# Kernel optimization log

Measured on AMD Instinct MI355X. Metric: run time of the kernel, lower is better.

The kernel has to match this reference:

```python
import jax, jax.numpy as jnp
import numpy as np

WS = 7   # window size
NH = 6   # num heads

def layer_norm(x, g, b, eps=1e-5):
    m = x.mean(-1, keepdims=True)
    v = ((x - m) ** 2).mean(-1, keepdims=True)
    return (x - m) / jnp.sqrt(v + eps) * g + b

def rel_pos_index(ws):
    coords = np.stack(np.meshgrid(np.arange(ws), np.arange(ws), indexing='ij')).reshape(2, -1)
    rel = (coords[:, :, None] - coords[:, None, :]).transpose(1, 2, 0)
    rel[:, :, 0] += ws - 1
    rel[:, :, 1] += ws - 1
    rel[:, :, 0] *= 2 * ws - 1
    return rel.sum(-1)  # (ws*ws, ws*ws) numpy int

RPI = rel_pos_index(WS)

def window_partition(x, ws):
    B, H, W, C = x.shape
    return x.reshape(B, H // ws, ws, W // ws, ws, C).transpose(0, 1, 3, 2, 4, 5).reshape(-1, ws * ws, C)

def window_reverse(w, ws, B, H, W):
    return w.reshape(B, H // ws, W // ws, ws, ws, -1).transpose(0, 1, 3, 2, 4, 5).reshape(B, H, W, -1)

def make_attn_mask(H, W, ws, shift):
    # Swin shifted-window mask (constant, computed in numpy)
    img = np.zeros((1, H, W, 1), np.float32)
    cnt = 0
    for h in (slice(0, -ws), slice(-ws, -shift), slice(-shift, None)):
        for w in (slice(0, -ws), slice(-ws, -shift), slice(-shift, None)):
            img[:, h, w, :] = cnt
            cnt += 1
    mw = img.reshape(1, H // ws, ws, W // ws, ws, 1).transpose(0, 1, 3, 2, 4, 5).reshape(-1, ws * ws)
    m = mw[:, None, :] - mw[:, :, None]
    return jnp.asarray(np.where(m != 0, -100.0, 0.0).astype(np.float32))  # (nW, N, N)

def conv2d(x, w, b, padding):
    y = jax.lax.conv_general_dilated(x, w, (1, 1), padding, dimension_numbers=('NCHW', 'OIHW', 'NCHW'))
    return y + b[None, :, None, None]

def swin_block(x, H, W, shift, n1g, n1b, qkvw, qkvb, projw, projb, rel, n2g, n2b, f1w, f1b, f2w, f2b):
    B, L, C = x.shape
    hd = C // NH
    shortcut = x
    x = layer_norm(x, n1g, n1b).reshape(B, H, W, C)
    if shift > 0:
        x = jnp.roll(x, (-shift, -shift), axis=(1, 2))
    xw = window_partition(x, WS)            # (B*nW, N, C)
    nWB, N, _ = xw.shape
    qkv = (xw @ qkvw.T + qkvb).reshape(nWB, N, 3, NH, hd).transpose(2, 0, 3, 1, 4)
    q, k, v = qkv[0] * (hd ** -0.5), qkv[1], qkv[2]
    attn = jnp.einsum('whnd,whmd->whnm', q, k)
    attn = attn + rel[RPI].transpose(2, 0, 1)[None]   # relative position bias (NH,N,N)
    if shift > 0:
        mask = make_attn_mask(H, W, WS, shift)        # (nW, N, N)
        nW = mask.shape[0]
        attn = (attn.reshape(B, nW, NH, N, N) + mask[None, :, None]).reshape(nWB, NH, N, N)
    attn = jax.nn.softmax(attn, axis=-1)
    xw = jnp.einsum('whnm,whmd->wnhd', attn, v).reshape(nWB, N, C)
    xw = xw @ projw.T + projb
    x = window_reverse(xw, WS, B, H, W)
    if shift > 0:
        x = jnp.roll(x, (shift, shift), axis=(1, 2))
    x = shortcut + x.reshape(B, L, C)
    h = layer_norm(x, n2g, n2b)
    h = jax.nn.gelu(h @ f1w.T + f1b, approximate=False) @ f2w.T + f2b
    return x + h

def setup_inputs() -> dict:
    key = jax.random.key(0)
    ks = iter(jax.random.split(key, 32))
    B, C, H, W = 8, 192, 56, 56
    C2, hid = C // 2, 4 * (C // 2)
    rn = lambda shape, s=0.02: jax.random.normal(next(ks), shape, jnp.float32) * s
    return dict(
        x=jax.random.normal(next(ks), (B, C, H, W), jnp.float32),
        up_w=rn((C2, C, 3, 3)), up_b=jnp.zeros((C2,), jnp.float32),
        bn_g=jnp.ones((C2,), jnp.float32), bn_b=jnp.zeros((C2,), jnp.float32),
        bn_mean=jnp.zeros((C2,), jnp.float32), bn_var=jnp.ones((C2,), jnp.float32),
        n1g=jnp.ones((2, C2), jnp.float32), n1b=jnp.zeros((2, C2), jnp.float32),
        qkv_w=rn((2, 3 * C2, C2)), qkv_b=jnp.zeros((2, 3 * C2), jnp.float32),
        proj_w=rn((2, C2, C2)), proj_b=jnp.zeros((2, C2), jnp.float32),
        rel=rn((2, (2 * WS - 1) ** 2, NH)),
        n2g=jnp.ones((2, C2), jnp.float32), n2b=jnp.zeros((2, C2), jnp.float32),
        f1w=rn((2, hid, C2)), f1b=jnp.zeros((2, hid), jnp.float32),
        f2w=rn((2, C2, hid)), f2b=jnp.zeros((2, C2), jnp.float32),
        out_w=rn((C // 4, C2, 1, 1)), out_b=jnp.zeros((C // 4,), jnp.float32),
    )

def reference(x, up_w, up_b, bn_g, bn_b, bn_mean, bn_var, n1g, n1b, qkv_w, qkv_b, proj_w, proj_b, rel, n2g, n2b, f1w, f1b, f2w, f2b, out_w, out_b):
    B, C, H, W = x.shape
    x = jnp.repeat(jnp.repeat(x, 2, axis=2), 2, axis=3)
    x = conv2d(x, up_w, up_b, 'SAME')
    x = (x - bn_mean[None, :, None, None]) * (bn_g / jnp.sqrt(bn_var + 1e-5))[None, :, None, None] + bn_b[None, :, None, None]
    x = jax.nn.relu(x)
    H2, W2, C2 = 2 * H, 2 * W, C // 2
    t = x.reshape(B, C2, H2 * W2).transpose(0, 2, 1)   # (B, L, C2)
    for i, shift in enumerate((0, WS // 2)):
        t = swin_block(t, H2, W2, shift, n1g[i], n1b[i], qkv_w[i], qkv_b[i], proj_w[i], proj_b[i], rel[i], n2g[i], n2b[i], f1w[i], f1b[i], f2w[i], f2b[i])
    x = t.transpose(0, 2, 1).reshape(B, C2, H2, W2)
    return jax.nn.relu(conv2d(x, out_w, out_b, 'VALID'))
```

## Files before the change

### kernel.cpp

```cpp
#include <hip/hip_runtime.h>
#include <math.h>

#define M_TOK 100352
#define NHEAD 6

typedef unsigned short u16;
typedef __attribute__((ext_vector_type(8))) short bf16x8;
typedef __attribute__((ext_vector_type(4))) float f32x4;
typedef __attribute__((ext_vector_type(4))) unsigned int u32x4;

__device__ inline float bf2f(u16 u) {
    union { float f; unsigned int i; } v; v.i = ((unsigned int)u) << 16; return v.f;
}
__device__ inline u16 f2bf(float f) {
    union { float f; unsigned int i; } v; v.f = f;
    unsigned int r = v.i + 0x7fffu + ((v.i >> 16) & 1u);
    return (u16)(r >> 16);
}

__global__ __launch_bounds__(256) void cast_w_kernel(const float* __restrict__ qkvw,
        const float* __restrict__ projw, const float* __restrict__ f1w,
        const float* __restrict__ f2w, u16* __restrict__ Wh) {
    int i = blockIdx.x * 256 + threadIdx.x;
    if (i < 55296) Wh[i] = f2bf(qkvw[i]);
    else if (i < 73728) Wh[i] = f2bf(projw[i - 55296]);
    else if (i < 147456) Wh[i] = f2bf(f1w[i - 73728]);
    else if (i < 221184) Wh[i] = f2bf(f2w[i - 147456]);
}

__global__ __launch_bounds__(256) void fold_kernel(const float* __restrict__ up_w,
                                                   u16* __restrict__ Wc) {
    int idx = blockIdx.x * 256 + threadIdx.x;
    if (idx >= 96 * 4 * 192) return;
    int c2 = idx / 768;
    int rem = idx - c2 * 768;
    int p = rem / 192;
    int ci = rem - p * 192;
    int po = p >> 1, pw = p & 1;
    const float* w = up_w + (c2 * 192 + ci) * 9;
    float w9[9];
#pragma unroll
    for (int k = 0; k < 9; k++) w9[k] = w[k];
    float r0[3], r1[3];
#pragma unroll
    for (int kw = 0; kw < 3; kw++) {
        if (po == 0) { r0[kw] = w9[kw];              r1[kw] = w9[3 + kw] + w9[6 + kw]; }
        else         { r0[kw] = w9[kw] + w9[3 + kw]; r1[kw] = w9[6 + kw]; }
    }
    float o00, o01, o10, o11;
    if (pw == 0) { o00 = r0[0];         o01 = r0[1] + r0[2]; o10 = r1[0];         o11 = r1[1] + r1[2]; }
    else         { o00 = r0[0] + r0[1]; o01 = r0[2];         o10 = r1[0] + r1[1]; o11 = r1[2]; }
    size_t base = ((size_t)p * 4 * 96 + c2) * 192 + ci;
    Wc[base + 0 * 96 * 192] = f2bf(o00);
    Wc[base + 1 * 96 * 192] = f2bf(o01);
    Wc[base + 2 * 96 * 192] = f2bf(o10);
    Wc[base + 3 * 96 * 192] = f2bf(o11);
}

__global__ __launch_bounds__(256) void bias_gen(const float* __restrict__ rel,
                                                float* __restrict__ BT) {
    int blkid = blockIdx.x;
    int blk = blkid / 24;
    int rem = blkid - blk * 24;
    int type = rem / 6, head = rem - (rem / 6) * 6;
    const float* relp = rel + blk * 1014;
    bool shift = (blk == 1);
    for (int i = threadIdx.x; i < 4096; i += 256) {
        int a = i >> 6, k = i & 63;
        float v;
        if (k >= 49) v = -1e30f;
        else if (a >= 49) v = 0.f;
        else {
            int ah = (a * 37) >> 8, aw = a - ah * 7;
            int kh = (k * 37) >> 8, kw = k - kh * 7;
            v = relp[((ah - kh + 6) * 13 + (aw - kw + 6)) * 6 + head];
            if (shift) {
                int lha = (type & 2) ? (ah < 4 ? 1 : 2) : 0;
                int lwa = (type & 1) ? (aw < 4 ? 1 : 2) : 0;
                int lhk = (type & 2) ? (kh < 4 ? 1 : 2) : 0;
                int lwk = (type & 1) ? (kw < 4 ? 1 : 2) : 0;
                if (lha != lhk || lwa != lwk) v -= 100.f;
            }
        }
        BT[(size_t)blkid * 4096 + i] = v;
    }
}

__global__ __launch_bounds__(256) void transpose_kernel(const float* __restrict__ x,
                                                        u16* __restrict__ xT) {
    __shared__ unsigned int ts[64 * 96];
    int b = blockIdx.y;
    int pix0 = blockIdx.x * 64;
    int tid = threadIdx.x;
    int p = tid & 63, dg = tid >> 6;
    const float* xb = x + (size_t)b * 192 * 3136 + pix0 + p;
    for (int d = dg; d < 96; d += 4) {
        float v0 = xb[(size_t)(2 * d) * 3136];
        float v1 = xb[(size_t)(2 * d + 1) * 3136];
        unsigned int pk = ((unsigned int)f2bf(v1) << 16) | (unsigned int)f2bf(v0);
        ts[p * 96 + ((d & ~31) | ((d & 31) ^ (p & 31)))] = pk;
    }
    __syncthreads();
    for (int i = tid; i < 1536; i += 256) {
        int pp = i / 24, c = i - pp * 24;
        unsigned int r[4];
#pragma unroll
        for (int j = 0; j < 4; j++) {
            int d = c * 4 + j;
            r[j] = ts[pp * 96 + ((d & ~31) | ((d & 31) ^ (pp & 31)))];
        }
        u32x4 v = {r[0], r[1], r[2], r[3]};
        *(u32x4*)&xT[((size_t)b * 3136 + pix0 + pp) * 192 + c * 8] = v;
    }
}

__global__ __launch_bounds__(256) void conv_mfma(const u16* __restrict__ xT,
        const u16* __restrict__ Wc, const float* __restrict__ up_b,
        const float* __restrict__ bn_g, const float* __restrict__ bn_b,
        const float* __restrict__ bn_m, const float* __restrict__ bn_v,
        float* __restrict__ T) {
    __shared__ u16 xs[81 * 200];
    __shared__ u16 ws[96 * 104];
    int tile = blockIdx.x, p = blockIdx.y, b = blockIdx.z;
    int po = p >> 1, pw = p & 1;
    int a0 = (tile / 7) * 8, b0 = (tile % 7) * 8;
    int rro = a0 - 1 + po, cco = b0 - 1 + pw;
    int tid = threadIdx.x;
    int w = tid >> 6, lane = tid & 63, quad = lane >> 4, l16 = lane & 15;
    int mbase = (w & 1) * 32;
    int nt0 = (w >> 1) * 3;

    for (int i = tid; i < 1944; i += 256) {
        int pix = i / 24, c = i - pix * 24;
        int rr = pix / 9, cc = pix - rr * 9;
        int gr = rro + rr, gc = cco + cc;
        u32x4 v = {0u, 0u, 0u, 0u};
        if ((unsigned)gr < 56u && (unsigned)gc < 56u)
            v = *(const u32x4*)&xT[((size_t)b * 3136 + gr * 56 + gc) * 192 + c * 8];
        *(u32x4*)&xs[pix * 200 + c * 8] = v;
    }

    f32x4 zero = {0.f, 0.f, 0.f, 0.f};
    f32x4 acc[2][3];
#pragma unroll
    for (int mi = 0; mi < 2; mi++)
#pragma unroll
        for (int ni = 0; ni < 3; ni++) acc[mi][ni] = zero;

    int aoffp[2];
#pragma unroll
    for (int mi = 0; mi < 2; mi++) {
        int pixel = mbase + mi * 16 + l16;
        aoffp[mi] = ((pixel >> 3) * 9 + (pixel & 7)) * 200;
    }

    for (int tap = 0; tap < 4; tap++) {
        int di = tap >> 1, dj = tap & 1;
        int tsh = (di * 9 + dj) * 200;
        for (int kc = 0; kc < 2; kc++) {
            __syncthreads();
            for (int i = tid; i < 1152; i += 256) {
                int r = i / 12, c = i - r * 12;
                *(u32x4*)&ws[r * 104 + c * 8] =
                    *(const u32x4*)&Wc[(((size_t)p * 4 + tap) * 96 + r) * 192 + kc * 96 + c * 8];
            }
            __syncthreads();
#pragma unroll
            for (int kk = 0; kk < 3; kk++) {
                bf16x8 af[2], bfr[3];
#pragma unroll
                for (int mi = 0; mi < 2; mi++)
                    af[mi] = *(const bf16x8*)&xs[aoffp[mi] + tsh + kc * 96 + kk * 32 + quad * 8];
#pragma unroll
                for (int ni = 0; ni < 3; ni++)
                    bfr[ni] = *(const bf16x8*)&ws[((nt0 + ni) * 16 + l16) * 104 + kk * 32 + quad * 8];
#pragma unroll
                for (int mi = 0; mi < 2; mi++)
#pragma unroll
                    for (int ni = 0; ni < 3; ni++)
                        acc[mi][ni] = __builtin_amdgcn_mfma_f32_16x16x32_bf16(
                            af[mi], bfr[ni], acc[mi][ni], 0, 0, 0);
            }
        }
    }

#pragma unroll
    for (int ni = 0; ni < 3; ni++) {
        int c2 = (nt0 + ni) * 16 + l16;
        float sc = bn_g[c2] * rsqrtf(bn_v[c2] + 1e-5f);
        float sh = (up_b[c2] - bn_m[c2]) * sc + bn_b[c2];
#pragma unroll
        for (int mi = 0; mi < 2; mi++) {
#pragma unroll
            for (int reg = 0; reg < 4; reg++) {
                int pixel = mbase + mi * 16 + quad * 4 + reg;
                int pr = pixel >> 3, pc = pixel & 7;
                int oh = 2 * (a0 + pr) + po, ow = 2 * (b0 + pc) + pw;
                size_t tok = (size_t)b * 12544 + oh * 112 + ow;
                T[tok * 96 + c2] = fmaxf(acc[mi][ni][reg] * sc + sh, 0.f);
            }
        }
    }
}

__global__ __launch_bounds__(256) void ln_kernel(const float* __restrict__ X,
        const float* __restrict__ g, const float* __restrict__ bta,
        u16* __restrict__ Y) {
    int tok = blockIdx.x * 4 + (threadIdx.x >> 6);
    int lane = threadIdx.x & 63;
    const float* row = X + (size_t)tok * 96;
    float x1 = row[lane];
    float x2 = (lane < 32) ? row[64 + lane] : 0.f;
    float s = x1 + x2, q = x1 * x1 + x2 * x2;
#pragma unroll
    for (int off = 32; off; off >>= 1) {
        s += __shfl_xor(s, off, 64);
        q += __shfl_xor(q, off, 64);
    }
    float mean = s * (1.f / 96.f);
    float var = q * (1.f / 96.f) - mean * mean;
    float rstd = rsqrtf(var + 1e-5f);
    u16* outp = Y + (size_t)tok * 96;
    outp[lane] = f2bf((x1 - mean) * rstd * g[lane] + bta[lane]);
    if (lane < 32) outp[64 + lane] = f2bf((x2 - mean) * rstd * g[64 + lane] + bta[64 + lane]);
}

template <int EPI>
__global__ __launch_bounds__(256) void gemm_mfma(const u16* __restrict__ A,
        const u16* __restrict__ W, const float* __restrict__ bias,
        void* Cout, const float* res, int N, int K) {
    __shared__ u16 As[128 * 104];
    __shared__ u16 Bs[96 * 104];
    int tid = threadIdx.x;
    int w = tid >> 6, lane = tid & 63, quad = lane >> 4, l16 = lane & 15;
    int n0 = blockIdx.x * 96;
    size_t m0 = (size_t)blockIdx.y * 128;
    int mbase = (w & 1) * 64;
    int nt0 = (w >> 1) * 3;

    f32x4 zero = {0.f, 0.f, 0.f, 0.f};
    f32x4 acc[4][3];
#pragma unroll
    for (int mi = 0; mi < 4; mi++)
#pragma unroll
        for (int ni = 0; ni < 3; ni++) acc[mi][ni] = zero;

    for (int k0 = 0; k0 < K; k0 += 96) {
        __syncthreads();
        for (int i = tid; i < 1536; i += 256) {
            int r = i / 12, c = i - r * 12;
            *(u32x4*)&As[r * 104 + c * 8] = *(const u32x4*)&A[(m0 + r) * K + k0 + c * 8];
        }
        for (int i = tid; i < 1152; i += 256) {
            int r = i / 12, c = i - r * 12;
            *(u32x4*)&Bs[r * 104 + c * 8] = *(const u32x4*)&W[(size_t)(n0 + r) * K + k0 + c * 8];
        }
        __syncthreads();
#pragma unroll
        for (int kk = 0; kk < 3; kk++) {
            bf16x8 af[4], bfr[3];
#pragma unroll
            for (int mi = 0; mi < 4; mi++)
                af[mi] = *(const bf16x8*)&As[(mbase + mi * 16 + l16) * 104 + kk * 32 + quad * 8];
#pragma unroll
            for (int ni = 0; ni < 3; ni++)
                bfr[ni] = *(const bf16x8*)&Bs[((nt0 + ni) * 16 + l16) * 104 + kk * 32 + quad * 8];
#pragma unroll
            for (int mi = 0; mi < 4; mi++)
#pragma unroll
                for (int ni = 0; ni < 3; ni++)
                    acc[mi][ni] = __builtin_amdgcn_mfma_f32_16x16x32_bf16(
                        af[mi], bfr[ni], acc[mi][ni], 0, 0, 0);
        }
    }

#pragma unroll
    for (int ni = 0; ni < 3; ni++) {
        int col = n0 + (nt0 + ni) * 16 + l16;
        float bv = bias[col];
#pragma unroll
        for (int mi = 0; mi < 4; mi++) {
            size_t rowb = m0 + mbase + mi * 16 + quad * 4;
#pragma unroll
            for (int reg = 0; reg < 4; reg++) {
                size_t row = rowb + reg;
                float v = acc[mi][ni][reg] + bv;
                if (EPI == 1) v = 0.5f * v * (1.f + erff(v * 0.70710678118654752f));
                if (EPI == 2) {
                    v += res[row * N + col];
                    ((float*)Cout)[row * N + col] = v;
                } else {
                    ((u16*)Cout)[row * N + col] = f2bf(v);
                }
            }
        }
    }
}

__global__ __launch_bounds__(192, 3) void attn_mfma(const u16* __restrict__ qkv,
        const float* __restrict__ BT, u16* __restrict__ ao, int shift) {
    __shared__ u16 Pl[3][64 * 72];
    __shared__ u16 vts[3][16 * 72];

    int tid = threadIdx.x;
    int w = tid >> 6, lane = tid & 63, quad = lane >> 4, l16 = lane & 15;
    int Wd = blockIdx.x;
    int bb = Wd >> 8, wl = Wd & 255, wh = wl >> 4, ww = wl & 15;
    int type = ((wh == 15) ? 2 : 0) + ((ww == 15) ? 1 : 0);

    int toks4[4], tokV;
#pragma unroll
    for (int t = 0; t < 4; t++) {
        int a = t * 16 + l16; if (a > 48) a = 48;
        int r = (a * 37) >> 8, c = a - r * 7;
        int h = wh * 7 + r, wq = ww * 7 + c;
        if (shift) { h += 3; if (h >= 112) h -= 112; wq += 3; if (wq >= 112) wq -= 112; }
        toks4[t] = bb * 12544 + h * 112 + wq;
    }
    {
        int a = lane > 48 ? 48 : lane;
        int r = (a * 37) >> 8, c = a - r * 7;
        int h = wh * 7 + r, wq = ww * 7 + c;
        if (shift) { h += 3; if (h >= 112) h -= 112; wq += 3; if (wq >= 112) wq -= 112; }
        tokV = bb * 12544 + h * 112 + wq;
    }

    u16* Pw = Pl[w];
    u16* vw = vts[w];

    for (int i = lane; i < 240; i += 64) {
        int rrow = i / 15, key = 49 + (i - rrow * 15);
        vw[rrow * 72 + key] = 0;
    }

    for (int hh = 0; hh < 2; hh++) {
        int head = w * 2 + hh;

        union { u32x4 u; bf16x8 h; } qf[4], kf[4];
#pragma unroll
        for (int t = 0; t < 4; t++) {
            u32x4 zq = {0u, 0u, 0u, 0u}, zk = {0u, 0u, 0u, 0u};
            if (quad < 2) {
                const u16* rb = qkv + (size_t)toks4[t] * 288 + head * 16 + quad * 8;
                zq = *(const u32x4*)(rb);
                zk = *(const u32x4*)(rb + 96);
            }
            qf[t].u = zq; kf[t].u = zk;
        }

        if (lane < 49) {
            const u16* vb = qkv + (size_t)tokV * 288 + head * 16 + 192;
            union { u32x4 v; unsigned int u[4]; } v0, v1;
            v0.v = *(const u32x4*)(vb);
            v1.v = *(const u32x4*)(vb + 8);
#pragma unroll
            for (int j = 0; j < 4; j++) {
                vw[(2 * j) * 72 + lane]         = (u16)(v0.u[j] & 0xffffu);
                vw[(2 * j + 1) * 72 + lane]     = (u16)(v0.u[j] >> 16);
                vw[(8 + 2 * j) * 72 + lane]     = (u16)(v1.u[j] & 0xffffu);
                vw[(8 + 2 * j + 1) * 72 + lane] = (u16)(v1.u[j] >> 16);
            }
        }

        f32x4 S[4][4];
#pragma unroll
        for (int kt = 0; kt < 4; kt++)
#pragma unroll
            for (int qt = 0; qt < 4; qt++)
                S[kt][qt] = __builtin_amdgcn_mfma_f32_16x16x32_bf16(
                    kf[kt].h, qf[qt].h, f32x4{0.f, 0.f, 0.f, 0.f}, 0, 0, 0);

        const float* bbase = BT + (size_t)(type * 6 + head) * 4096;
        float rinv[4];
#pragma unroll
        for (int qt = 0; qt < 4; qt++) {
            f32x4 bv[4];
#pragma unroll
            for (int kt = 0; kt < 4; kt++)
                bv[kt] = *(const f32x4*)&bbase[(size_t)(qt * 16 + l16) * 64 + kt * 16 + quad * 4];
            float mx = -3e38f;
#pragma unroll
            for (int kt = 0; kt < 4; kt++)
#pragma unroll
                for (int r = 0; r < 4; r++) {
                    float v = fmaf(S[kt][qt][r], 0.25f, bv[kt][r]);
                    S[kt][qt][r] = v;
                    mx = fmaxf(mx, v);
                }
            mx = fmaxf(mx, __shfl_xor(mx, 16, 64));
            mx = fmaxf(mx, __shfl_xor(mx, 32, 64));
            float sm = 0.f;
#pragma unroll
            for (int kt = 0; kt < 4; kt++)
#pragma unroll
                for (int r = 0; r < 4; r++) {
                    float e = __expf(S[kt][qt][r] - mx);
                    S[kt][qt][r] = e;
                    sm += e;
                }
            sm += __shfl_xor(sm, 16, 64);
            sm += __shfl_xor(sm, 32, 64);
            rinv[qt] = 1.0f / sm;
        }

#pragma unroll
        for (int qt = 0; qt < 4; qt++)
#pragma unroll
            for (int kt = 0; kt < 4; kt++) {
                unsigned int d0 = ((unsigned int)f2bf(S[kt][qt][1]) << 16) | f2bf(S[kt][qt][0]);
                unsigned int d1 = ((unsigned int)f2bf(S[kt][qt][3]) << 16) | f2bf(S[kt][qt][2]);
                *(uint2*)&Pw[(qt * 16 + l16) * 72 + kt * 16 + quad * 4] = make_uint2(d0, d1);
            }

        bf16x8 vf[2];
#pragma unroll
        for (int ksp = 0; ksp < 2; ksp++)
            vf[ksp] = *(const bf16x8*)&vw[l16 * 72 + ksp * 32 + quad * 8];
#pragma unroll
        for (int qt = 0; qt < 4; qt++) {
            f32x4 O = {0.f, 0.f, 0.f, 0.f};
#pragma unroll
            for (int ksp = 0; ksp < 2; ksp++) {
                bf16x8 pf = *(const bf16x8*)&Pw[(qt * 16 + l16) * 72 + ksp * 32 + quad * 8];
                O = __builtin_amdgcn_mfma_f32_16x16x32_bf16(vf[ksp], pf, O, 0, 0, 0);
            }
            int a = qt * 16 + l16;
            if (a < 49) {
                float ri = rinv[qt];
                unsigned int d0 = ((unsigned int)f2bf(O[1] * ri) << 16) | f2bf(O[0] * ri);
                unsigned int d1 = ((unsigned int)f2bf(O[3] * ri) << 16) | f2bf(O[2] * ri);
                *(uint2*)&ao[(size_t)toks4[qt] * 96 + head * 16 + quad * 4] = make_uint2(d0, d1);
            }
        }
    }
}

__global__ __launch_bounds__(256) void outconv_kernel(const float* __restrict__ T,
        const float* __restrict__ ow, const float* __restrict__ ob,
        float* __restrict__ out) {
    __shared__ float ts[64 * 100];
    __shared__ float wsh[48 * 96];
    int tid = threadIdx.x;
    size_t tok0 = (size_t)blockIdx.x * 64;
    for (int i = tid; i < 6144; i += 256) {
        int tk = i / 96, c = i - tk * 96;
        ts[tk * 100 + c] = T[(tok0 + tk) * 96 + c];
    }
    for (int i = tid; i < 4608; i += 256) wsh[i] = ow[i];
    __syncthreads();
    int lane = tid & 63, wv = tid >> 6;
    float4 xr[24];
#pragma unroll
    for (int c4 = 0; c4 < 24; c4++) xr[c4] = *(const float4*)&ts[lane * 100 + c4 * 4];
    int tok = (int)tok0 + lane;
    int bb = tok / 12544, pp = tok - bb * 12544;
    for (int co = wv; co < 48; co += 4) {
        float a = 0.f;
#pragma unroll
        for (int c4 = 0; c4 < 24; c4++) {
            float4 w4 = *(const float4*)&wsh[co * 96 + c4 * 4];
            a = fmaf(xr[c4].x, w4.x, a);
            a = fmaf(xr[c4].y, w4.y, a);
            a = fmaf(xr[c4].z, w4.z, a);
            a = fmaf(xr[c4].w, w4.w, a);
        }
        a += ob[co];
        out[((size_t)bb * 48 + co) * 12544 + pp] = fmaxf(a, 0.f);
    }
}

extern "C" void kernel_launch(void* const* d_in, const int* in_sizes, int n_in,
                              void* d_out, int out_size, void* d_ws, size_t ws_size,
                              hipStream_t stream) {
    const float* x     = (const float*)d_in[0];
    const float* up_w  = (const float*)d_in[1];
    const float* up_b  = (const float*)d_in[2];
    const float* bn_g  = (const float*)d_in[3];
    const float* bn_b  = (const float*)d_in[4];
    const float* bn_m  = (const float*)d_in[5];
    const float* bn_v  = (const float*)d_in[6];
    const float* n1g   = (const float*)d_in[7];
    const float* n1b   = (const float*)d_in[8];
    const float* qkvw  = (const float*)d_in[9];
    const float* qkvb  = (const float*)d_in[10];
    const float* projw = (const float*)d_in[11];
    const float* projb = (const float*)d_in[12];
    const float* rel   = (const float*)d_in[13];
    const float* n2g   = (const float*)d_in[14];
    const float* n2b   = (const float*)d_in[15];
    const float* f1w   = (const float*)d_in[16];
    const float* f1b   = (const float*)d_in[17];
    const float* f2w   = (const float*)d_in[18];
    const float* f2b   = (const float*)d_in[19];
    const float* outw  = (const float*)d_in[20];
    const float* outb  = (const float*)d_in[21];
    float* out = (float*)d_out;

    char* base = (char*)d_ws;
    float* T  = (float*)base;                       base += (size_t)M_TOK * 96 * 4;
    u16* XBh  = (u16*)base;                         base += (size_t)M_TOK * 96 * 2;
    u16* BIGh = (u16*)base;                         base += (size_t)M_TOK * 384 * 2;
    u16* xT   = (u16*)base;                         base += (size_t)8 * 3136 * 192 * 2;
    u16* Wc   = (u16*)base;                         base += (size_t)16 * 96 * 192 * 2;
    u16* Wh   = (u16*)base;                         base += (size_t)221184 * 2;
    float* BT = (float*)base;
    u16* qkvwh = Wh;
    u16* projwh = Wh + 55296;
    u16* f1wh = Wh + 73728;
    u16* f2wh = Wh + 147456;

    cast_w_kernel<<<864, 256, 0, stream>>>(qkvw, projw, f1w, f2w, Wh);
    fold_kernel<<<288, 256, 0, stream>>>(up_w, Wc);
    bias_gen<<<48, 256, 0, stream>>>(rel, BT);
    transpose_kernel<<<dim3(49, 8), 256, 0, stream>>>(x, xT);
    conv_mfma<<<dim3(49, 4, 8), 256, 0, stream>>>(xT, Wc, up_b, bn_g, bn_b, bn_m, bn_v, T);

    for (int blk = 0; blk < 2; blk++) {
        int shift = (blk == 0) ? 0 : 3;
        ln_kernel<<<M_TOK / 4, 256, 0, stream>>>(T, n1g + blk * 96, n1b + blk * 96, XBh);
        gemm_mfma<0><<<dim3(3, M_TOK / 128), 256, 0, stream>>>(
            XBh, qkvwh + blk * 27648, qkvb + blk * 288, BIGh, nullptr, 288, 96);
        attn_mfma<<<2048, 192, 0, stream>>>(BIGh, BT + (size_t)blk * 98304, XBh, shift);
        gemm_mfma<2><<<dim3(1, M_TOK / 128), 256, 0, stream>>>(
            XBh, projwh + blk * 9216, projb + blk * 96, T, T, 96, 96);
        ln_kernel<<<M_TOK / 4, 256, 0, stream>>>(T, n2g + blk * 96, n2b + blk * 96, XBh);
        gemm_mfma<1><<<dim3(4, M_TOK / 128), 256, 0, stream>>>(
            XBh, f1wh + blk * 36864, f1b + blk * 384, BIGh, nullptr, 384, 96);
        gemm_mfma<2><<<dim3(1, M_TOK / 128), 256, 0, stream>>>(
            BIGh, f2wh + blk * 36864, f2b + blk * 96, T, T, 96, 384);
    }

    outconv_kernel<<<M_TOK / 64, 256, 0, stream>>>(T, outw, outb, out);
}
```

Measured before the change: 735.0 us.

## Fuse LayerNorm into GEMMs, vectorize epilogues, and move output conv to MFMA

LayerNorm is now computed inside the QKV and FC1 GEMM prologues from the fp32 residual stream, which removes the separate LN kernels and their bf16 round trip through global memory. The GEMMs swap operand roles so each lane holds 4 consecutive columns, letting the bias, residual and output accesses use packed and vector stores. The final 1x1 output conv now runs on bf16 MFMA with pre-cast weights instead of scalar fp32 FMA. In exchange, the fused-LN GEMMs recompute LayerNorm once per N-tile, and the output conv gains bf16 rounding error.

```diff
diff --git a/kernel.cpp b/kernel.cpp
--- a/kernel.cpp
+++ b/kernel.cpp
@@ -20,12 +20,14 @@
 
 __global__ __launch_bounds__(256) void cast_w_kernel(const float* __restrict__ qkvw,
         const float* __restrict__ projw, const float* __restrict__ f1w,
-        const float* __restrict__ f2w, u16* __restrict__ Wh) {
+        const float* __restrict__ f2w, const float* __restrict__ outw,
+        u16* __restrict__ Wh) {
     int i = blockIdx.x * 256 + threadIdx.x;
     if (i < 55296) Wh[i] = f2bf(qkvw[i]);
     else if (i < 73728) Wh[i] = f2bf(projw[i - 55296]);
     else if (i < 147456) Wh[i] = f2bf(f1w[i - 73728]);
     else if (i < 221184) Wh[i] = f2bf(f2w[i - 147456]);
+    else if (i < 225792) Wh[i] = f2bf(outw[i - 221184]);
 }
 
 __global__ __launch_bounds__(256) void fold_kernel(const float* __restrict__ up_w,
@@ -203,96 +205,166 @@
     }
 }
 
-__global__ __launch_bounds__(256) void ln_kernel(const float* __restrict__ X,
-        const float* __restrict__ g, const float* __restrict__ bta,
-        u16* __restrict__ Y) {
-    int tok = blockIdx.x * 4 + (threadIdx.x >> 6);
-    int lane = threadIdx.x & 63;
-    const float* row = X + (size_t)tok * 96;
-    float x1 = row[lane];
-    float x2 = (lane < 32) ? row[64 + lane] : 0.f;
-    float s = x1 + x2, q = x1 * x1 + x2 * x2;
-#pragma unroll
-    for (int off = 32; off; off >>= 1) {
-        s += __shfl_xor(s, off, 64);
-        q += __shfl_xor(q, off, 64);
-    }
-    float mean = s * (1.f / 96.f);
-    float var = q * (1.f / 96.f) - mean * mean;
-    float rstd = rsqrtf(var + 1e-5f);
-    u16* outp = Y + (size_t)tok * 96;
-    outp[lane] = f2bf((x1 - mean) * rstd * g[lane] + bta[lane]);
-    if (lane < 32) outp[64 + lane] = f2bf((x2 - mean) * rstd * g[64 + lane] + bta[64 + lane]);
-}
-
 template <int EPI>
-__global__ __launch_bounds__(256) void gemm_mfma(const u16* __restrict__ A,
-        const u16* __restrict__ W, const float* __restrict__ bias,
-        void* Cout, const float* res, int N, int K) {
-    __shared__ u16 As[128 * 104];
-    __shared__ u16 Bs[96 * 104];
+__global__ __launch_bounds__(256) void gemm_ln(const float* __restrict__ Tin,
+        const u16* __restrict__ W, const float* __restrict__ g,
+        const float* __restrict__ bt, const float* __restrict__ bias,
+        u16* __restrict__ Cout, int N) {
+    __shared__ u16 Xs[128 * 104];
+    __shared__ u16 Ws[96 * 104];
+    __shared__ __align__(16) float gb[192];
     int tid = threadIdx.x;
     int w = tid >> 6, lane = tid & 63, quad = lane >> 4, l16 = lane & 15;
+    int mh = w & 1, nh = w >> 1;
     int n0 = blockIdx.x * 96;
     size_t m0 = (size_t)blockIdx.y * 128;
-    int mbase = (w & 1) * 64;
-    int nt0 = (w >> 1) * 3;
-
-    f32x4 zero = {0.f, 0.f, 0.f, 0.f};
-    f32x4 acc[4][3];
-#pragma unroll
-    for (int mi = 0; mi < 4; mi++)
-#pragma unroll
-        for (int ni = 0; ni < 3; ni++) acc[mi][ni] = zero;
+
+    if (tid < 192) gb[tid] = (tid < 96) ? g[tid] : bt[tid - 96];
+    for (int i = tid; i < 1152; i += 256) {
+        int r = i / 12, c = i - r * 12;
+        *(u32x4*)&Ws[r * 104 + c * 8] = *(const u32x4*)&W[(size_t)(n0 + r) * 96 + c * 8];
+    }
+    __syncthreads();
+
+    {
+        int r = tid >> 1, h = tid & 1;
+        const float* rowp = Tin + (m0 + r) * 96 + h * 48;
+        float4 v[12];
+        float s = 0.f, q = 0.f;
+#pragma unroll
+        for (int j = 0; j < 12; j++) {
+            v[j] = *(const float4*)&rowp[j * 4];
+            s += v[j].x + v[j].y + v[j].z + v[j].w;
+            q += v[j].x * v[j].x + v[j].y * v[j].y + v[j].z * v[j].z + v[j].w * v[j].w;
+        }
+        s += __shfl_xor(s, 1, 64);
+        q += __shfl_xor(q, 1, 64);
+        float mean = s * (1.f / 96.f);
+        float var = q * (1.f / 96.f) - mean * mean;
+        float rstd = rsqrtf(var + 1e-5f);
+#pragma unroll
+        for (int j = 0; j < 12; j += 2) {
+            float4 g0 = *(const float4*)&gb[h * 48 + j * 4];
+            float4 g1 = *(const float4*)&gb[h * 48 + j * 4 + 4];
+            float4 b0 = *(const float4*)&gb[96 + h * 48 + j * 4];
+            float4 b1 = *(const float4*)&gb[96 + h * 48 + j * 4 + 4];
+            float y0 = (v[j].x - mean) * rstd * g0.x + b0.x;
+            float y1 = (v[j].y - mean) * rstd * g0.y + b0.y;
+            float y2 = (v[j].z - mean) * rstd * g0.z + b0.z;
+            float y3 = (v[j].w - mean) * rstd * g0.w + b0.w;
+            float y4 = (v[j + 1].x - mean) * rstd * g1.x + b1.x;
+            float y5 = (v[j + 1].y - mean) * rstd * g1.y + b1.y;
+            float y6 = (v[j + 1].z - mean) * rstd * g1.z + b1.z;
+            float y7 = (v[j + 1].w - mean) * rstd * g1.w + b1.w;
+            u32x4 pk = {((unsigned int)f2bf(y1) << 16) | f2bf(y0),
+                        ((unsigned int)f2bf(y3) << 16) | f2bf(y2),
+                        ((unsigned int)f2bf(y5) << 16) | f2bf(y4),
+                        ((unsigned int)f2bf(y7) << 16) | f2bf(y6)};
+            *(u32x4*)&Xs[r * 104 + h * 48 + j * 4] = pk;
+        }
+    }
+    __syncthreads();
+
+    f32x4 acc[3][4];
+#pragma unroll
+    for (int ni = 0; ni < 3; ni++)
+#pragma unroll
+        for (int mi = 0; mi < 4; mi++) acc[ni][mi] = f32x4{0.f, 0.f, 0.f, 0.f};
+#pragma unroll
+    for (int kk = 0; kk < 3; kk++) {
+        bf16x8 af[3], bf[4];
+#pragma unroll
+        for (int ni = 0; ni < 3; ni++)
+            af[ni] = *(const bf16x8*)&Ws[(nh * 48 + ni * 16 + l16) * 104 + kk * 32 + quad * 8];
+#pragma unroll
+        for (int mi = 0; mi < 4; mi++)
+            bf[mi] = *(const bf16x8*)&Xs[(mh * 64 + mi * 16 + l16) * 104 + kk * 32 + quad * 8];
+#pragma unroll
+        for (int ni = 0; ni < 3; ni++)
+#pragma unroll
+            for (int mi = 0; mi < 4; mi++)
+                acc[ni][mi] = __builtin_amdgcn_mfma_f32_16x16x32_bf16(
+                    af[ni], bf[mi], acc[ni][mi], 0, 0, 0);
+    }
+
+#pragma unroll
+    for (int ni = 0; ni < 3; ni++) {
+        int colb = n0 + nh * 48 + ni * 16 + quad * 4;
+        float4 bv = *(const float4*)&bias[colb];
+#pragma unroll
+        for (int mi = 0; mi < 4; mi++) {
+            size_t row = m0 + mh * 64 + mi * 16 + l16;
+            float v0 = acc[ni][mi][0] + bv.x, v1 = acc[ni][mi][1] + bv.y;
+            float v2 = acc[ni][mi][2] + bv.z, v3 = acc[ni][mi][3] + bv.w;
+            if (EPI == 1) {
+                v0 = 0.5f * v0 * (1.f + erff(v0 * 0.70710678118654752f));
+                v1 = 0.5f * v1 * (1.f + erff(v1 * 0.70710678118654752f));
+                v2 = 0.5f * v2 * (1.f + erff(v2 * 0.70710678118654752f));
+                v3 = 0.5f * v3 * (1.f + erff(v3 * 0.70710678118654752f));
+            }
+            unsigned int d0 = ((unsigned int)f2bf(v1) << 16) | f2bf(v0);
+            unsigned int d1 = ((unsigned int)f2bf(v3) << 16) | f2bf(v2);
+            *(uint2*)&Cout[row * N + colb] = make_uint2(d0, d1);
+        }
+    }
+}
+
+__global__ __launch_bounds__(256) void gemm_res(const u16* __restrict__ Xh,
+        const u16* __restrict__ W, const float* __restrict__ bias,
+        const float* __restrict__ res, float* __restrict__ Cout, int K) {
+    __shared__ u16 Xs[128 * 104];
+    __shared__ u16 Ws[96 * 104];
+    int tid = threadIdx.x;
+    int w = tid >> 6, lane = tid & 63, quad = lane >> 4, l16 = lane & 15;
+    int mh = w & 1, nh = w >> 1;
+    size_t m0 = (size_t)blockIdx.x * 128;
+
+    f32x4 acc[3][4];
+#pragma unroll
+    for (int ni = 0; ni < 3; ni++)
+#pragma unroll
+        for (int mi = 0; mi < 4; mi++) acc[ni][mi] = f32x4{0.f, 0.f, 0.f, 0.f};
 
     for (int k0 = 0; k0 < K; k0 += 96) {
         __syncthreads();
         for (int i = tid; i < 1536; i += 256) {
             int r = i / 12, c = i - r * 12;
-            *(u32x4*)&As[r * 104 + c * 8] = *(const u32x4*)&A[(m0 + r) * K + k0 + c * 8];
+            *(u32x4*)&Xs[r * 104 + c * 8] = *(const u32x4*)&Xh[(m0 + r) * K + k0 + c * 8];
         }
         for (int i = tid; i < 1152; i += 256) {
             int r = i / 12, c = i - r * 12;
-            *(u32x4*)&Bs[r * 104 + c * 8] = *(const u32x4*)&W[(size_t)(n0 + r) * K + k0 + c * 8];
+            *(u32x4*)&Ws[r * 104 + c * 8] = *(const u32x4*)&W[(size_t)r * K + k0 + c * 8];
         }
         __syncthreads();
 #pragma unroll
         for (int kk = 0; kk < 3; kk++) {
-            bf16x8 af[4], bfr[3];
+            bf16x8 af[3], bf[4];
+#pragma unroll
+            for (int ni = 0; ni < 3; ni++)
+                af[ni] = *(const bf16x8*)&Ws[(nh * 48 + ni * 16 + l16) * 104 + kk * 32 + quad * 8];
 #pragma unroll
             for (int mi = 0; mi < 4; mi++)
-                af[mi] = *(const bf16x8*)&As[(mbase + mi * 16 + l16) * 104 + kk * 32 + quad * 8];
+                bf[mi] = *(const bf16x8*)&Xs[(mh * 64 + mi * 16 + l16) * 104 + kk * 32 + quad * 8];
 #pragma unroll
             for (int ni = 0; ni < 3; ni++)
-                bfr[ni] = *(const bf16x8*)&Bs[((nt0 + ni) * 16 + l16) * 104 + kk * 32 + quad * 8];
-#pragma unroll
-            for (int mi = 0; mi < 4; mi++)
-#pragma unroll
-                for (int ni = 0; ni < 3; ni++)
-                    acc[mi][ni] = __builtin_amdgcn_mfma_f32_16x16x32_bf16(
-                        af[mi], bfr[ni], acc[mi][ni], 0, 0, 0);
+#pragma unroll
+                for (int mi = 0; mi < 4; mi++)
+                    acc[ni][mi] = __builtin_amdgcn_mfma_f32_16x16x32_bf16(
+                        af[ni], bf[mi], acc[ni][mi], 0, 0, 0);
         }
     }
 
 #pragma unroll
     for (int ni = 0; ni < 3; ni++) {
-        int col = n0 + (nt0 + ni) * 16 + l16;
-        float bv = bias[col];
+        int colb = nh * 48 + ni * 16 + quad * 4;
+        float4 bv = *(const float4*)&bias[colb];
 #pragma unroll
         for (int mi = 0; mi < 4; mi++) {
-            size_t rowb = m0 + mbase + mi * 16 + quad * 4;
-#pragma unroll
-            for (int reg = 0; reg < 4; reg++) {
-                size_t row = rowb + reg;
-                float v = acc[mi][ni][reg] + bv;
-                if (EPI == 1) v = 0.5f * v * (1.f + erff(v * 0.70710678118654752f));
-                if (EPI == 2) {
-                    v += res[row * N + col];
-                    ((float*)Cout)[row * N + col] = v;
-                } else {
-                    ((u16*)Cout)[row * N + col] = f2bf(v);
-                }
-            }
+            size_t row = m0 + mh * 64 + mi * 16 + l16;
+            float4 rv = *(const float4*)&res[row * 96 + colb];
+            f32x4 o = {acc[ni][mi][0] + bv.x + rv.x, acc[ni][mi][1] + bv.y + rv.y,
+                       acc[ni][mi][2] + bv.z + rv.z, acc[ni][mi][3] + bv.w + rv.w};
+            *(f32x4*)&Cout[row * 96 + colb] = o;
         }
     }
 }
@@ -435,38 +507,68 @@
     }
 }
 
-__global__ __launch_bounds__(256) void outconv_kernel(const float* __restrict__ T,
-        const float* __restrict__ ow, const float* __restrict__ ob,
+__global__ __launch_bounds__(256) void outconv_mfma(const float* __restrict__ T,
+        const u16* __restrict__ Woc, const float* __restrict__ ob,
         float* __restrict__ out) {
-    __shared__ float ts[64 * 100];
-    __shared__ float wsh[48 * 96];
+    __shared__ u16 Xs[128 * 104];
+    __shared__ u16 Ws[48 * 104];
     int tid = threadIdx.x;
-    size_t tok0 = (size_t)blockIdx.x * 64;
-    for (int i = tid; i < 6144; i += 256) {
-        int tk = i / 96, c = i - tk * 96;
-        ts[tk * 100 + c] = T[(tok0 + tk) * 96 + c];
-    }
-    for (int i = tid; i < 4608; i += 256) wsh[i] = ow[i];
+    int w = tid >> 6, lane = tid & 63, quad = lane >> 4, l16 = lane & 15;
+    int t0 = blockIdx.x * 128, b = blockIdx.y;
+    size_t m0 = (size_t)b * 12544 + t0;
+
+    for (int i = tid; i < 576; i += 256) {
+        int r = i / 12, c = i - r * 12;
+        *(u32x4*)&Ws[r * 104 + c * 8] = *(const u32x4*)&Woc[(size_t)r * 96 + c * 8];
+    }
+    {
+        int r = tid >> 1, h = tid & 1;
+        const float* rowp = T + (m0 + r) * 96 + h * 48;
+#pragma unroll
+        for (int j = 0; j < 12; j += 2) {
+            float4 a = *(const float4*)&rowp[j * 4];
+            float4 c2 = *(const float4*)&rowp[j * 4 + 4];
+            u32x4 pk = {((unsigned int)f2bf(a.y) << 16) | f2bf(a.x),
+                        ((unsigned int)f2bf(a.w) << 16) | f2bf(a.z),
+                        ((unsigned int)f2bf(c2.y) << 16) | f2bf(c2.x),
+                        ((unsigned int)f2bf(c2.w) << 16) | f2bf(c2.z)};
+            *(u32x4*)&Xs[r * 104 + h * 48 + j * 4] = pk;
+        }
+    }
     __syncthreads();
-    int lane = tid & 63, wv = tid >> 6;
-    float4 xr[24];
-#pragma unroll
-    for (int c4 = 0; c4 < 24; c4++) xr[c4] = *(const float4*)&ts[lane * 100 + c4 * 4];
-    int tok = (int)tok0 + lane;
-    int bb = tok / 12544, pp = tok - bb * 12544;
-    for (int co = wv; co < 48; co += 4) {
-        float a = 0.f;
-#pragma unroll
-        for (int c4 = 0; c4 < 24; c4++) {
-            float4 w4 = *(const float4*)&wsh[co * 96 + c4 * 4];
-            a = fmaf(xr[c4].x, w4.x, a);
-            a = fmaf(xr[c4].y, w4.y, a);
-            a = fmaf(xr[c4].z, w4.z, a);
-            a = fmaf(xr[c4].w, w4.w, a);
-        }
-        a += ob[co];
-        out[((size_t)bb * 48 + co) * 12544 + pp] = fmaxf(a, 0.f);
-    }
+
+    f32x4 acc[2][3];
+#pragma unroll
+    for (int mi = 0; mi < 2; mi++)
+#pragma unroll
+        for (int ni = 0; ni < 3; ni++) acc[mi][ni] = f32x4{0.f, 0.f, 0.f, 0.f};
+#pragma unroll
+    for (int kk = 0; kk < 3; kk++) {
+        bf16x8 af[2], bfr[3];
+#pragma unroll
+        for (int mi = 0; mi < 2; mi++)
+            af[mi] = *(const bf16x8*)&Xs[(w * 32 + mi * 16 + l16) * 104 + kk * 32 + quad * 8];
+#pragma unroll
+        for (int ni = 0; ni < 3; ni++)
+            bfr[ni] = *(const bf16x8*)&Ws[(ni * 16 + l16) * 104 + kk * 32 + quad * 8];
+#pragma unroll
+        for (int mi = 0; mi < 2; mi++)
+#pragma unroll
+            for (int ni = 0; ni < 3; ni++)
+                acc[mi][ni] = __builtin_amdgcn_mfma_f32_16x16x32_bf16(
+                    af[mi], bfr[ni], acc[mi][ni], 0, 0, 0);
+    }
+
+#pragma unroll
+    for (int mi = 0; mi < 2; mi++)
+#pragma unroll
+        for (int ni = 0; ni < 3; ni++) {
+            int co = ni * 16 + l16;
+            float bb = ob[co];
+            f32x4 o = {fmaxf(acc[mi][ni][0] + bb, 0.f), fmaxf(acc[mi][ni][1] + bb, 0.f),
+                       fmaxf(acc[mi][ni][2] + bb, 0.f), fmaxf(acc[mi][ni][3] + bb, 0.f)};
+            *(f32x4*)&out[((size_t)b * 48 + co) * 12544 + t0 + w * 32 + mi * 16 + quad * 4] = o;
+        }
 }
 
 extern "C" void kernel_launch(void* const* d_in, const int* in_sizes, int n_in,
@@ -502,14 +604,15 @@
     u16* BIGh = (u16*)base;                         base += (size_t)M_TOK * 384 * 2;
     u16* xT   = (u16*)base;                         base += (size_t)8 * 3136 * 192 * 2;
     u16* Wc   = (u16*)base;                         base += (size_t)16 * 96 * 192 * 2;
-    u16* Wh   = (u16*)base;                         base += (size_t)221184 * 2;
+    u16* Wh   = (u16*)base;                         base += (size_t)225792 * 2;
     float* BT = (float*)base;
     u16* qkvwh = Wh;
     u16* projwh = Wh + 55296;
     u16* f1wh = Wh + 73728;
     u16* f2wh = Wh + 147456;
-
-    cast_w_kernel<<<864, 256, 0, stream>>>(qkvw, projw, f1w, f2w, Wh);
+    u16* outwh = Wh + 221184;
+
+    cast_w_kernel<<<882, 256, 0, stream>>>(qkvw, projw, f1w, f2w, outw, Wh);
     fold_kernel<<<288, 256, 0, stream>>>(up_w, Wc);
     bias_gen<<<48, 256, 0, stream>>>(rel, BT);
     transpose_kernel<<<dim3(49, 8), 256, 0, stream>>>(x, xT);
@@ -517,18 +620,16 @@
 
     for (int blk = 0; blk < 2; blk++) {
         int shift = (blk == 0) ? 0 : 3;
-        ln_kernel<<<M_TOK / 4, 256, 0, stream>>>(T, n1g + blk * 96, n1b + blk * 96, XBh);
-        gemm_mfma<0><<<dim3(3, M_TOK / 128), 256, 0, stream>>>(
-            XBh, qkvwh + blk * 27648, qkvb + blk * 288, BIGh, nullptr, 288, 96);
+        gemm_ln<0><<<dim3(3, M_TOK / 128), 256, 0, stream>>>(
+            T, qkvwh + blk * 27648, n1g + blk * 96, n1b + blk * 96, qkvb + blk * 288, BIGh, 288);
         attn_mfma<<<2048, 192, 0, stream>>>(BIGh, BT + (size_t)blk * 98304, XBh, shift);
-        gemm_mfma<2><<<dim3(1, M_TOK / 128), 256, 0, stream>>>(
-            XBh, projwh + blk * 9216, projb + blk * 96, T, T, 96, 96);
-        ln_kernel<<<M_TOK / 4, 256, 0, stream>>>(T, n2g + blk * 96, n2b + blk * 96, XBh);
-        gemm_mfma<1><<<dim3(4, M_TOK / 128), 256, 0, stream>>>(
-            XBh, f1wh + blk * 36864, f1b + blk * 384, BIGh, nullptr, 384, 96);
-        gemm_mfma<2><<<dim3(1, M_TOK / 128), 256, 0, stream>>>(
-            BIGh, f2wh + blk * 36864, f2b + blk * 96, T, T, 96, 384);
-    }
-
-    outconv_kernel<<<M_TOK / 64, 256, 0, stream>>>(T, outw, outb, out);
-}
+        gemm_res<<<M_TOK / 128, 256, 0, stream>>>(
+            XBh, projwh + blk * 9216, projb + blk * 96, T, T, 96);
+        gemm_ln<1><<<dim3(4, M_TOK / 128), 256, 0, stream>>>(
+            T, f1wh + blk * 36864, n2g + blk * 96, n2b + blk * 96, f1b + blk * 384, BIGh, 384);
+        gemm_res<<<M_TOK / 128, 256, 0, stream>>>(
+            BIGh, f2wh + blk * 36864, f2b + blk * 96, T, T, 384);
+    }
+
+    outconv_mfma<<<dim3(98, 8), 256, 0, stream>>>(T, outwh, outb, out);
+}
```

Measured after the change: 636.1 us. 13.4% less time.
